# Optimization experiments

Hardware: AMD Instinct MI355X
Metric: run time of the kernel (lower is better)

The kernel has to match this reference:

```python
import jax, jax.numpy as jnp
import numpy as np

N = 200000   # active voxel sites
G = 80       # voxel grid extent per axis
K = 27       # 3x3x3 kernel offsets
CIN = 64
COUT = 128
EPS = 1e-5


def _build_rulebook(seed=0):
    """Submanifold 3x3x3 rulebook: for each offset k and output site i,
    in_idx[k,i] = index of neighbor site (or 0 if absent),
    out_idx[k,i] = i (or N = dummy row if neighbor absent)."""
    rng = np.random.default_rng(seed)
    lin = rng.choice(G ** 3, size=N, replace=False).astype(np.int64)
    lut = np.full(G ** 3, -1, dtype=np.int64)
    lut[lin] = np.arange(N)
    cx, cy, cz = lin // (G * G), (lin // G) % G, lin % G
    offs = [(dx, dy, dz) for dx in (-1, 0, 1) for dy in (-1, 0, 1) for dz in (-1, 0, 1)]
    in_idx = np.zeros((K, N), np.int32)
    out_idx = np.full((K, N), N, np.int32)
    ar = np.arange(N, dtype=np.int32)
    for k, (dx, dy, dz) in enumerate(offs):
        nx, ny, nz = cx + dx, cy + dy, cz + dz
        ok = (nx >= 0) & (nx < G) & (ny >= 0) & (ny < G) & (nz >= 0) & (nz < G)
        nb_lin = np.where(ok, nx * G * G + ny * G + nz, 0)
        j = lut[nb_lin]
        valid = ok & (j >= 0)
        in_idx[k] = np.where(valid, j, 0).astype(np.int32)
        out_idx[k] = np.where(valid, ar, N)
    return jnp.asarray(in_idx), jnp.asarray(out_idx)


def setup_inputs() -> dict:
    key = jax.random.key(0)
    ks = jax.random.split(key, 8)
    in_idx, out_idx = _build_rulebook(0)
    s1 = 1.0 / np.sqrt(CIN * K)
    s2 = 1.0 / np.sqrt(COUT * K)
    ss = 1.0 / np.sqrt(CIN)
    return {
        "feats": jax.random.normal(ks[0], (N, CIN), jnp.float32),
        "in_idx": in_idx,
        "out_idx": out_idx,
        "W1": jax.random.normal(ks[1], (K, CIN, COUT), jnp.float32) * s1,
        "g1": jnp.ones((COUT,), jnp.float32) + 0.1 * jax.random.normal(ks[2], (COUT,), jnp.float32),
        "b1": 0.1 * jax.random.normal(ks[3], (COUT,), jnp.float32),
        "W2": jax.random.normal(ks[4], (K, COUT, COUT), jnp.float32) * s2,
        "g2": jnp.ones((COUT,), jnp.float32) + 0.1 * jax.random.normal(ks[5], (COUT,), jnp.float32),
        "b2": 0.1 * jax.random.normal(ks[6], (COUT,), jnp.float32),
        "Wsc": jax.random.normal(ks[7], (CIN, COUT), jnp.float32) * ss,
        "gsc": jnp.ones((COUT,), jnp.float32),
        "bsc": jnp.zeros((COUT,), jnp.float32),
    }


def _spconv(feats, W, in_idx, out_idx):
    """Rulebook gather-GEMM-scatter sparse conv. feats [N,Cin], W [K,Cin,Cout]."""
    cout = W.shape[-1]
    out = jnp.zeros((N + 1, cout), feats.dtype)  # row N = dummy for padded pairs
    for k in range(K):  # fixed small structural loop over kernel offsets
        out = out.at[out_idx[k]].add(feats[in_idx[k]] @ W[k])
    return out[:N]


def _bn(x, gamma, beta):
    # training-mode BatchNorm over the site dimension (biased variance)
    m = jnp.mean(x, axis=0)
    v = jnp.var(x, axis=0)
    return (x - m) * jax.lax.rsqrt(v + EPS) * gamma + beta


def reference(feats, in_idx, out_idx, W1, g1, b1, W2, g2, b2, Wsc, gsc, bsc):
    h = jax.nn.relu(_bn(_spconv(feats, W1, in_idx, out_idx), g1, b1))
    h = _bn(_spconv(h, W2, in_idx, out_idx), g2, b2)
    sc = _bn(feats @ Wsc, gsc, bsc)  # 1x1 sparse conv == per-site linear
    return jax.nn.relu(h + sc)
```

## Files before the change

kernel.cpp:

```cpp
#include <hip/hip_runtime.h>

#define NS 200000
#define NK 27
#define NB 782
#define NBSC 1563
#define EPSV 1e-5f

typedef __bf16 bf16x8 __attribute__((ext_vector_type(8)));
typedef float f32x4 __attribute__((ext_vector_type(4)));
typedef unsigned short u16;
typedef u16 u16x8 __attribute__((ext_vector_type(8)));
typedef u16 u16x4 __attribute__((ext_vector_type(4)));
typedef unsigned u32;

__device__ __forceinline__ u16 f2bf(float f) {
  union { float f; unsigned u; } v; v.f = f;
  unsigned r = v.u + 0x7fffu + ((v.u >> 16) & 1u);
  return (u16)(r >> 16);
}
__device__ __forceinline__ float bf2f(u16 u) {
  union { unsigned u; float f; } v; v.u = ((unsigned)u) << 16;
  return v.f;
}

__global__ void k_prep_all(const float* __restrict__ feats,
                           const int* __restrict__ in_idx, const int* __restrict__ out_idx,
                           const float* __restrict__ W1, const float* __restrict__ W2,
                           const float* __restrict__ Wsc,
                           u16* __restrict__ Xbf, int* __restrict__ gidx,
                           u16* __restrict__ Wp1, u16* __restrict__ Wp2,
                           u16* __restrict__ Wpsc, float* __restrict__ stats) {
  long i = (long)blockIdx.x * 256 + threadIdx.x;
  if (i < 768) stats[i] = 0.f;
  if (i < (long)NS * 64) Xbf[i] = f2bf(feats[i]);
  if (i < (long)NK * NS) gidx[i] = (out_idx[i] != NS) ? in_idx[i] : NS;
  const int n1 = NK * 64 * 128, n2 = NK * 128 * 128, n3 = 64 * 128;
  if (i < (long)(n1 + n2 + n3)) {
    int ii = (int)i;
    const float* src; u16* dst; int f, S, C;
    if (ii < n1)           { src = W1;  dst = Wp1;  f = ii;           S = 2; C = 64; }
    else if (ii < n1 + n2) { src = W2;  dst = Wp2;  f = ii - n1;      S = 4; C = 128; }
    else                   { src = Wsc; dst = Wpsc; f = ii - n1 - n2; S = 2; C = 64; }
    int j = f & 7, l = (f >> 3) & 63, cf = (f >> 9) & 7;
    int rest = f >> 12;
    int s = rest % S, k = rest / S;
    int kk = s * 32 + (l >> 4) * 8 + j;
    dst[f] = f2bf(src[(k * C + kk) * 128 + cf * 16 + (l & 15)]);
  }
}

template <int C>
__global__ __launch_bounds__(256, 2) void k_conv(
    const u16* __restrict__ X, const u16* __restrict__ Wp,
    const int* __restrict__ gidx,
    u16* __restrict__ Y, float* __restrict__ partial) {
  constexpr int S = C / 32;
  constexpr int SLICE = C * 128;
  constexpr int NST = C / 16;
  constexpr int WAITN = NST + 4;
  __shared__ alignas(16) u16 Wbuf[2 * SLICE];
  __shared__ float red[1024];

  const int t = threadIdx.x, w = t >> 6, l = t & 63;
  const int lr = l & 15, lh = l >> 4;
  const int rowbase = blockIdx.x * 256 + w * 64;
  const int laneoff = l * 8;

  int rc[4]; bool ok[4];
  #pragma unroll
  for (int m = 0; m < 4; ++m) {
    int r = rowbase + m * 16 + lr;
    ok[m] = r < NS;
    rc[m] = ok[m] ? r : 0;
  }

  auto stage = [&](int k, int p) {
    #pragma unroll
    for (int i = 0; i < NST; ++i) {
      const u16* g = Wp + k * SLICE + (w * NST + i) * 512 + laneoff;
      u16* d = &Wbuf[p * SLICE + (w * NST + i) * 512];
      __builtin_amdgcn_global_load_lds(
          (const __attribute__((address_space(1))) u32*)g,
          (__attribute__((address_space(3))) u32*)d, 16, 0, 0);
    }
  };
  auto loadidx = [&](int k, int (&dst)[4]) {
    #pragma unroll
    for (int m = 0; m < 4; ++m) {
      int v = gidx[k * NS + rc[m]];
      dst[m] = ok[m] ? v : NS;
    }
  };
  auto gather = [&](const int (&src)[4], bf16x8 (&a)[4][S]) {
    #pragma unroll
    for (int m = 0; m < 4; ++m) {
      #pragma unroll
      for (int s = 0; s < S; ++s) a[m][s] = bf16x8{};
      if (src[m] != NS) {
        const u16* rowp = X + src[m] * C + lh * 8;
        #pragma unroll
        for (int s = 0; s < S; ++s)
          a[m][s] = *reinterpret_cast<const bf16x8*>(rowp + s * 32);
      }
    }
  };
  auto compute = [&](int p, const bf16x8 (&a)[4][S], f32x4 (&ac)[4][8]) {
    __builtin_amdgcn_s_setprio(1);
    #pragma unroll
    for (int s = 0; s < S; ++s)
      #pragma unroll
      for (int cf = 0; cf < 8; ++cf) {
        bf16x8 b = *reinterpret_cast<const bf16x8*>(
            &Wbuf[p * SLICE + (s * 8 + cf) * 512 + laneoff]);
        #pragma unroll
        for (int m = 0; m < 4; ++m)
          ac[m][cf] = __builtin_amdgcn_mfma_f32_16x16x32_bf16(a[m][s], b, ac[m][cf], 0, 0, 0);
      }
    __builtin_amdgcn_s_setprio(0);
  };

  f32x4 acc[4][8];
  #pragma unroll
  for (int m = 0; m < 4; ++m)
    #pragma unroll
    for (int cf = 0; cf < 8; ++cf) acc[m][cf] = (f32x4){0.f, 0.f, 0.f, 0.f};

  bf16x8 av[4][S];
  int sv0[4], sv1[4];

  loadidx(0, sv0);
  stage(0, 0);
  loadidx(1, sv1);
  gather(sv0, av);

  #pragma unroll 1
  for (int k = 0; k < NK - 1; k += 2) {
    stage(k + 1, 1);
    loadidx(k + 2, sv0);
    asm volatile("s_waitcnt vmcnt(%0)\n\ts_barrier" :: "i"(WAITN) : "memory");
    compute(0, av, acc);
    gather(sv1, av);
    asm volatile("s_waitcnt lgkmcnt(0)\n\ts_barrier" ::: "memory");
    stage(k + 2, 0);
    { int kn = (k + 3 < NK) ? k + 3 : NK - 1; loadidx(kn, sv1); }
    asm volatile("s_waitcnt vmcnt(%0)\n\ts_barrier" :: "i"(WAITN) : "memory");
    compute(1, av, acc);
    gather(sv0, av);
    asm volatile("s_waitcnt lgkmcnt(0)\n\ts_barrier" ::: "memory");
  }
  asm volatile("s_waitcnt vmcnt(0)\n\ts_barrier" ::: "memory");
  compute(0, av, acc);

  #pragma unroll
  for (int m = 0; m < 4; ++m)
    #pragma unroll
    for (int cf = 0; cf < 8; ++cf) {
      int ch = cf * 16 + lr;
      #pragma unroll
      for (int r = 0; r < 4; ++r) {
        int row = rowbase + m * 16 + lh * 4 + r;
        if (row < NS) Y[row * 128 + ch] = f2bf(acc[m][cf][r]);
      }
    }
  #pragma unroll
  for (int cf = 0; cf < 8; ++cf) {
    float s = 0.f, q = 0.f;
    #pragma unroll
    for (int m = 0; m < 4; ++m)
      #pragma unroll
      for (int r = 0; r < 4; ++r) { float v = acc[m][cf][r]; s += v; q += v * v; }
    s += __shfl_xor(s, 16); s += __shfl_xor(s, 32);
    q += __shfl_xor(q, 16); q += __shfl_xor(q, 32);
    if (lh == 0) {
      red[w * 256 + cf * 16 + lr] = s;
      red[w * 256 + 128 + cf * 16 + lr] = q;
    }
  }
  __syncthreads();
  if (t < 256)
    partial[blockIdx.x * 256 + t] =
        red[t] + red[256 + t] + red[512 + t] + red[768 + t];
}

__global__ __launch_bounds__(256, 2) void k_sc(
    const u16* __restrict__ X, const u16* __restrict__ Wpsc,
    u16* __restrict__ SCb, float* __restrict__ partial) {
  __shared__ float red[1024];
  const int t = threadIdx.x, w = t >> 6, l = t & 63;
  const int lr = l & 15, lh = l >> 4;
  const int rowbase = blockIdx.x * 128 + w * 32;
  const int laneoff = l * 8;

  bf16x8 ai[2][2];
  #pragma unroll
  for (int m = 0; m < 2; ++m) {
    int r = rowbase + m * 16 + lr;
    #pragma unroll
    for (int s = 0; s < 2; ++s) ai[m][s] = bf16x8{};
    if (r < NS) {
      const u16* rowp = X + r * 64 + lh * 8;
      ai[m][0] = *reinterpret_cast<const bf16x8*>(rowp);
      ai[m][1] = *reinterpret_cast<const bf16x8*>(rowp + 32);
    }
  }
  f32x4 acc[2][8];
  #pragma unroll
  for (int m = 0; m < 2; ++m)
    #pragma unroll
    for (int cf = 0; cf < 8; ++cf) acc[m][cf] = (f32x4){0.f, 0.f, 0.f, 0.f};
  #pragma unroll
  for (int s = 0; s < 2; ++s)
    #pragma unroll
    for (int cf = 0; cf < 8; ++cf) {
      bf16x8 b = *reinterpret_cast<const bf16x8*>(Wpsc + (s * 8 + cf) * 512 + laneoff);
      acc[0][cf] = __builtin_amdgcn_mfma_f32_16x16x32_bf16(ai[0][s], b, acc[0][cf], 0, 0, 0);
      acc[1][cf] = __builtin_amdgcn_mfma_f32_16x16x32_bf16(ai[1][s], b, acc[1][cf], 0, 0, 0);
    }
  #pragma unroll
  for (int m = 0; m < 2; ++m)
    #pragma unroll
    for (int cf = 0; cf < 8; ++cf) {
      int ch = cf * 16 + lr;
      #pragma unroll
      for (int r = 0; r < 4; ++r) {
        int row = rowbase + m * 16 + lh * 4 + r;
        if (row < NS) SCb[row * 128 + ch] = f2bf(acc[m][cf][r]);
      }
    }
  #pragma unroll
  for (int cf = 0; cf < 8; ++cf) {
    float s = 0.f, q = 0.f;
    #pragma unroll
    for (int m = 0; m < 2; ++m)
      #pragma unroll
      for (int r = 0; r < 4; ++r) { float v = acc[m][cf][r]; s += v; q += v * v; }
    s += __shfl_xor(s, 16); s += __shfl_xor(s, 32);
    q += __shfl_xor(q, 16); q += __shfl_xor(q, 32);
    if (lh == 0) {
      red[w * 256 + cf * 16 + lr] = s;
      red[w * 256 + 128 + cf * 16 + lr] = q;
    }
  }
  __syncthreads();
  if (t < 256)
    partial[(long)blockIdx.x * 256 + t] =
        red[t] + red[256 + t] + red[512 + t] + red[768 + t];
}

__global__ void k_red1x2(const float* __restrict__ pa, const float* __restrict__ pb,
                         float* __restrict__ tmp) {
  int c = threadIdx.x;
  const float* p = (blockIdx.x == 0) ? pa : pb;
  int nrows = (blockIdx.x == 0) ? NB : NBSC;
  int roff  = (blockIdx.x == 0) ? 0 : 256;
  float s = 0.f;
  for (int r = blockIdx.y; r < nrows; r += 32) s += p[(long)r * 256 + c];
  tmp[(long)blockIdx.y * 512 + roff + c] = s;
}
__global__ void k_red1(const float* __restrict__ part, float* __restrict__ tmp,
                       int nrows) {
  int c = threadIdx.x;
  float s = 0.f;
  for (int r = blockIdx.y; r < nrows; r += 32) s += part[(long)r * 256 + c];
  tmp[(long)blockIdx.y * 512 + c] = s;
}
__global__ void k_red2(const float* __restrict__ tmp, float* __restrict__ out) {
  int c = blockIdx.x * 256 + threadIdx.x;
  float s = 0.f;
  #pragma unroll
  for (int r = 0; r < 32; ++r) s += tmp[(long)r * 512 + c];
  out[c] = s;
}

__global__ void k_bnrelu(const u16* __restrict__ Y1, const float* __restrict__ stats,
                         const float* __restrict__ g, const float* __restrict__ b,
                         u16* __restrict__ H) {
  long i8 = (long)blockIdx.x * 256 + threadIdx.x;
  const long tot = (long)NS * 16;
  if (i8 >= tot) return;
  int ch0 = ((int)i8 & 15) * 8;
  u16x8 y = *reinterpret_cast<const u16x8*>(Y1 + i8 * 8);
  u16x8 o;
  #pragma unroll
  for (int e = 0; e < 8; ++e) {
    int ch = ch0 + e;
    float m = stats[ch] * (1.f / NS);
    float var = stats[128 + ch] * (1.f / NS) - m * m;
    float a = g[ch] * rsqrtf(var + EPSV);
    float bb = b[ch] - m * a;
    float h = bf2f(y[e]) * a + bb;
    o[e] = f2bf(h > 0.f ? h : 0.f);
  }
  *reinterpret_cast<u16x8*>(H + i8 * 8) = o;
}

__global__ void k_final(const u16* __restrict__ Y2, const u16* __restrict__ SCb,
                        const float* __restrict__ stats,
                        const float* __restrict__ g2, const float* __restrict__ b2,
                        const float* __restrict__ gsc, const float* __restrict__ bsc,
                        float* __restrict__ out) {
  long i8 = (long)blockIdx.x * 256 + threadIdx.x;
  if (i8 >= (long)NS * 16) return;
  int ch0 = ((int)i8 & 15) * 8;
  u16x8 y = *reinterpret_cast<const u16x8*>(Y2 + i8 * 8);
  u16x8 s = *reinterpret_cast<const u16x8*>(SCb + i8 * 8);
  f32x4 o0, o1;
  #pragma unroll
  for (int e = 0; e < 8; ++e) {
    int ch = ch0 + e;
    float m2 = stats[512 + ch] * (1.f / NS);
    float v2 = stats[640 + ch] * (1.f / NS) - m2 * m2;
    float a2 = g2[ch] * rsqrtf(v2 + EPSV);
    float msc = stats[256 + ch] * (1.f / NS);
    float vsc = stats[384 + ch] * (1.f / NS) - msc * msc;
    float asc = gsc[ch] * rsqrtf(vsc + EPSV);
    float val = bf2f(y[e]) * a2 + (b2[ch] - m2 * a2)
              + bf2f(s[e]) * asc + (bsc[ch] - msc * asc);
    float rv = val > 0.f ? val : 0.f;
    if (e < 4) o0[e] = rv; else o1[e - 4] = rv;
  }
  *reinterpret_cast<f32x4*>(out + i8 * 8) = o0;
  *reinterpret_cast<f32x4*>(out + i8 * 8 + 4) = o1;
}

extern "C" void kernel_launch(void* const* d_in, const int* in_sizes, int n_in,
                              void* d_out, int out_size, void* d_ws, size_t ws_size,
                              hipStream_t stream) {
  const float* feats = (const float*)d_in[0];
  const int* in_idx  = (const int*)d_in[1];
  const int* out_idx = (const int*)d_in[2];
  const float* W1  = (const float*)d_in[3];
  const float* g1  = (const float*)d_in[4];
  const float* b1  = (const float*)d_in[5];
  const float* W2  = (const float*)d_in[6];
  const float* g2  = (const float*)d_in[7];
  const float* b2  = (const float*)d_in[8];
  const float* Wsc = (const float*)d_in[9];
  const float* gsc = (const float*)d_in[10];
  const float* bsc = (const float*)d_in[11];

  char* ws = (char*)d_ws;
  size_t off = 0;
  auto alloc = [&](size_t bytes) {
    void* p = ws + off; off += (bytes + 255) & ~(size_t)255; return p;
  };
  float* stats = (float*)alloc(768 * 4);
  float* rtmp  = (float*)alloc(32 * 512 * 4);
  u16* Xbf  = (u16*)alloc((size_t)NS * 64 * 2);
  u16* SCbf = (u16*)alloc((size_t)NS * 128 * 2);
  u16* Hbf  = (u16*)alloc((size_t)NS * 128 * 2);
  u16* Y2bf = (u16*)alloc((size_t)NS * 128 * 2);
  u16* Wp1  = (u16*)alloc((size_t)NK * 64 * 128 * 2);
  u16* Wp2  = (u16*)alloc((size_t)NK * 128 * 128 * 2);
  u16* Wpsc = (u16*)alloc((size_t)64 * 128 * 2);
  u16* Y1bf = (u16*)d_out;
  int* gidx = (int*)((char*)d_out + (size_t)NS * 128 * 2);
  float* part1  = (float*)Y2bf;
  float* partsc = part1 + (size_t)NB * 256;
  float* part2  = (float*)Xbf;

  hipLaunchKernelGGL(k_prep_all, dim3(50000), dim3(256), 0, stream,
                     feats, in_idx, out_idx, W1, W2, Wsc,
                     Xbf, gidx, Wp1, Wp2, Wpsc, stats);
  hipLaunchKernelGGL(k_sc, dim3(NBSC), dim3(256), 0, stream, Xbf, Wpsc, SCbf, partsc);
  hipLaunchKernelGGL((k_conv<64>), dim3(NB), dim3(256), 0, stream,
                     Xbf, Wp1, gidx, Y1bf, part1);
  hipLaunchKernelGGL(k_red1x2, dim3(2, 32), dim3(256), 0, stream, part1, partsc, rtmp);
  hipLaunchKernelGGL(k_red2, dim3(2), dim3(256), 0, stream, rtmp, stats);
  hipLaunchKernelGGL(k_bnrelu, dim3(12500), dim3(256), 0, stream, Y1bf, stats, g1, b1, Hbf);
  hipLaunchKernelGGL((k_conv<128>), dim3(NB), dim3(256), 0, stream,
                     Hbf, Wp2, gidx, Y2bf, part2);
  hipLaunchKernelGGL(k_red1, dim3(1, 32), dim3(256), 0, stream, part2, rtmp, NB);
  hipLaunchKernelGGL(k_red2, dim3(1), dim3(256), 0, stream, rtmp, stats + 512);
  hipLaunchKernelGGL(k_final, dim3(12500), dim3(256), 0, stream,
                     Y2bf, SCbf, stats, g2, b2, gsc, bsc, (float*)d_out);
}
```

Measured before the change: 421.4 us.

## Stage gathered activation rows into LDS via async loads with 2D warp tiling

The sparse conv kernel now gathers neighbor rows straight into a swizzled LDS buffer with global_load_lds, double-buffered with the weights, so gathers no longer go through registers. Blocks grow to 512 threads over 128 rows, and each wave owns a 64x32 output tile (wm/wn split), which shrinks accumulator registers and allows more occupancy. Absent neighbors now point to a zeroed dummy row NS in X and H instead of being masked per lane, which needs extra padding rows and tail handling. The added LDS use and the new synchronization pattern may limit the occupancy this is meant to gain.

```diff
diff --git a/kernel.cpp b/kernel.cpp
--- a/kernel.cpp
+++ b/kernel.cpp
@@ -2,15 +2,13 @@
 
 #define NS 200000
 #define NK 27
-#define NB 782
-#define NBSC 1563
+#define NB 1563
 #define EPSV 1e-5f
 
 typedef __bf16 bf16x8 __attribute__((ext_vector_type(8)));
 typedef float f32x4 __attribute__((ext_vector_type(4)));
 typedef unsigned short u16;
 typedef u16 u16x8 __attribute__((ext_vector_type(8)));
-typedef u16 u16x4 __attribute__((ext_vector_type(4)));
 typedef unsigned u32;
 
 __device__ __forceinline__ u16 f2bf(float f) {
@@ -32,6 +30,7 @@
                            u16* __restrict__ Wpsc, float* __restrict__ stats) {
   long i = (long)blockIdx.x * 256 + threadIdx.x;
   if (i < 768) stats[i] = 0.f;
+  if (i < 64 && blockIdx.x == 0) Xbf[(long)NS * 64 + i] = (u16)0;
   if (i < (long)NS * 64) Xbf[i] = f2bf(feats[i]);
   if (i < (long)NK * NS) gidx[i] = (out_idx[i] != NS) ? in_idx[i] : NS;
   const int n1 = NK * 64 * 128, n2 = NK * 128 * 128, n3 = 64 * 128;
@@ -50,136 +49,148 @@
 }
 
 template <int C>
-__global__ __launch_bounds__(256, 2) void k_conv(
+__global__ __launch_bounds__(512, (C == 64) ? 4 : 2) void k_conv(
     const u16* __restrict__ X, const u16* __restrict__ Wp,
     const int* __restrict__ gidx,
     u16* __restrict__ Y, float* __restrict__ partial) {
   constexpr int S = C / 32;
-  constexpr int SLICE = C * 128;
-  constexpr int NST = C / 16;
-  constexpr int WAITN = NST + 4;
-  __shared__ alignas(16) u16 Wbuf[2 * SLICE];
-  __shared__ float red[1024];
+  constexpr int UA = C / 8;
+  constexpr int LUA = (C == 64) ? 3 : 4;
+  constexpr int ASL = 128 * UA * 8;
+  constexpr int WSL = C * 128;
+  constexpr int NIT = (C == 64) ? 2 : 4;
+  constexpr int RPI = 512 >> LUA;
+  constexpr int WAITN = 3 * NIT;
+  __shared__ alignas(16) u16 Wbuf[2 * WSL];
+  __shared__ alignas(16) u16 Abuf[2 * ASL];
+  __shared__ float red[512];
 
   const int t = threadIdx.x, w = t >> 6, l = t & 63;
   const int lr = l & 15, lh = l >> 4;
-  const int rowbase = blockIdx.x * 256 + w * 64;
-  const int laneoff = l * 8;
-
-  int rc[4]; bool ok[4];
-  #pragma unroll
-  for (int m = 0; m < 4; ++m) {
-    int r = rowbase + m * 16 + lr;
-    ok[m] = r < NS;
-    rc[m] = ok[m] ? r : 0;
-  }
-
-  auto stage = [&](int k, int p) {
-    #pragma unroll
-    for (int i = 0; i < NST; ++i) {
-      const u16* g = Wp + k * SLICE + (w * NST + i) * 512 + laneoff;
-      u16* d = &Wbuf[p * SLICE + (w * NST + i) * 512];
+  const int wm = w >> 2, wn = w & 3;
+  const int rowblk = blockIdx.x * 128;
+
+  auto stageW = [&](int k, int p) {
+    #pragma unroll
+    for (int i = 0; i < NIT; ++i) {
+      const u16* g = Wp + (long)k * WSL + (i * 512 + t) * 8;
+      u16* d = &Wbuf[p * WSL + (i * 512 + t) * 8];
       __builtin_amdgcn_global_load_lds(
           (const __attribute__((address_space(1))) u32*)g,
           (__attribute__((address_space(3))) u32*)d, 16, 0, 0);
     }
   };
-  auto loadidx = [&](int k, int (&dst)[4]) {
-    #pragma unroll
-    for (int m = 0; m < 4; ++m) {
-      int v = gidx[k * NS + rc[m]];
-      dst[m] = ok[m] ? v : NS;
-    }
-  };
-  auto gather = [&](const int (&src)[4], bf16x8 (&a)[4][S]) {
-    #pragma unroll
-    for (int m = 0; m < 4; ++m) {
-      #pragma unroll
-      for (int s = 0; s < S; ++s) a[m][s] = bf16x8{};
-      if (src[m] != NS) {
-        const u16* rowp = X + src[m] * C + lh * 8;
-        #pragma unroll
-        for (int s = 0; s < S; ++s)
-          a[m][s] = *reinterpret_cast<const bf16x8*>(rowp + s * 32);
+  auto loadidx = [&](int k, int (&iv)[NIT]) {
+    #pragma unroll
+    for (int i = 0; i < NIT; ++i) {
+      int rg = rowblk + i * RPI + (t >> LUA);
+      bool okr = rg < NS;
+      int v = gidx[(long)k * NS + (okr ? rg : 0)];
+      iv[i] = okr ? v : NS;
+    }
+  };
+  auto stageA = [&](int p, const int (&iv)[NIT]) {
+    #pragma unroll
+    for (int i = 0; i < NIT; ++i) {
+      int rloc = i * RPI + (t >> LUA);
+      int c = t & (UA - 1);
+      int csw = c ^ (rloc & 7);
+      const u16* g = X + (long)iv[i] * C + csw * 8;
+      u16* d = &Abuf[p * ASL + ((i * 512 + t) * 8)];
+      __builtin_amdgcn_global_load_lds(
+          (const __attribute__((address_space(1))) u32*)g,
+          (__attribute__((address_space(3))) u32*)d, 16, 0, 0);
+    }
+  };
+  auto compute = [&](int p, f32x4 (&ac)[4][2]) {
+    __builtin_amdgcn_s_setprio(1);
+    #pragma unroll
+    for (int s = 0; s < S; ++s) {
+      bf16x8 a[4];
+      #pragma unroll
+      for (int m = 0; m < 4; ++m) {
+        int row = wm * 64 + m * 16 + lr;
+        int unit = row * UA + ((s * 4 + lh) ^ (row & 7));
+        a[m] = *reinterpret_cast<const bf16x8*>(&Abuf[p * ASL + unit * 8]);
       }
-    }
-  };
-  auto compute = [&](int p, const bf16x8 (&a)[4][S], f32x4 (&ac)[4][8]) {
-    __builtin_amdgcn_s_setprio(1);
-    #pragma unroll
-    for (int s = 0; s < S; ++s)
-      #pragma unroll
-      for (int cf = 0; cf < 8; ++cf) {
+      #pragma unroll
+      for (int nf = 0; nf < 2; ++nf) {
         bf16x8 b = *reinterpret_cast<const bf16x8*>(
-            &Wbuf[p * SLICE + (s * 8 + cf) * 512 + laneoff]);
+            &Wbuf[p * WSL + (s * 8 + wn * 2 + nf) * 512 + l * 8]);
         #pragma unroll
         for (int m = 0; m < 4; ++m)
-          ac[m][cf] = __builtin_amdgcn_mfma_f32_16x16x32_bf16(a[m][s], b, ac[m][cf], 0, 0, 0);
+          ac[m][nf] = __builtin_amdgcn_mfma_f32_16x16x32_bf16(a[m], b, ac[m][nf], 0, 0, 0);
       }
+    }
     __builtin_amdgcn_s_setprio(0);
   };
 
-  f32x4 acc[4][8];
+  f32x4 acc[4][2];
   #pragma unroll
   for (int m = 0; m < 4; ++m)
     #pragma unroll
-    for (int cf = 0; cf < 8; ++cf) acc[m][cf] = (f32x4){0.f, 0.f, 0.f, 0.f};
-
-  bf16x8 av[4][S];
-  int sv0[4], sv1[4];
+    for (int nf = 0; nf < 2; ++nf) acc[m][nf] = (f32x4){0.f, 0.f, 0.f, 0.f};
+
+  int sv0[NIT], sv1[NIT];
 
   loadidx(0, sv0);
-  stage(0, 0);
   loadidx(1, sv1);
-  gather(sv0, av);
+  stageW(0, 0);
+  asm volatile("s_waitcnt vmcnt(%0)" :: "i"(2 * NIT) : "memory");
+  stageA(0, sv0);
 
   #pragma unroll 1
   for (int k = 0; k < NK - 1; k += 2) {
-    stage(k + 1, 1);
+    stageW(k + 1, 1);
     loadidx(k + 2, sv0);
+    asm volatile("s_waitcnt vmcnt(%0)" :: "i"(WAITN) : "memory");
+    stageA(1, sv1);
     asm volatile("s_waitcnt vmcnt(%0)\n\ts_barrier" :: "i"(WAITN) : "memory");
-    compute(0, av, acc);
-    gather(sv1, av);
+    compute(0, acc);
     asm volatile("s_waitcnt lgkmcnt(0)\n\ts_barrier" ::: "memory");
-    stage(k + 2, 0);
+    stageW(k + 2, 0);
     { int kn = (k + 3 < NK) ? k + 3 : NK - 1; loadidx(kn, sv1); }
+    asm volatile("s_waitcnt vmcnt(%0)" :: "i"(WAITN) : "memory");
+    stageA(0, sv0);
     asm volatile("s_waitcnt vmcnt(%0)\n\ts_barrier" :: "i"(WAITN) : "memory");
-    compute(1, av, acc);
-    gather(sv0, av);
+    compute(1, acc);
     asm volatile("s_waitcnt lgkmcnt(0)\n\ts_barrier" ::: "memory");
   }
   asm volatile("s_waitcnt vmcnt(0)\n\ts_barrier" ::: "memory");
-  compute(0, av, acc);
+  compute(0, acc);
 
   #pragma unroll
   for (int m = 0; m < 4; ++m)
     #pragma unroll
-    for (int cf = 0; cf < 8; ++cf) {
-      int ch = cf * 16 + lr;
+    for (int nf = 0; nf < 2; ++nf) {
+      int ch = wn * 32 + nf * 16 + lr;
       #pragma unroll
       for (int r = 0; r < 4; ++r) {
-        int row = rowbase + m * 16 + lh * 4 + r;
-        if (row < NS) Y[row * 128 + ch] = f2bf(acc[m][cf][r]);
+        int row = rowblk + wm * 64 + m * 16 + lh * 4 + r;
+        if (row < NS) Y[(long)row * 128 + ch] = f2bf(acc[m][nf][r]);
       }
     }
   #pragma unroll
-  for (int cf = 0; cf < 8; ++cf) {
+  for (int nf = 0; nf < 2; ++nf) {
     float s = 0.f, q = 0.f;
     #pragma unroll
     for (int m = 0; m < 4; ++m)
       #pragma unroll
-      for (int r = 0; r < 4; ++r) { float v = acc[m][cf][r]; s += v; q += v * v; }
+      for (int r = 0; r < 4; ++r) { float v = acc[m][nf][r]; s += v; q += v * v; }
     s += __shfl_xor(s, 16); s += __shfl_xor(s, 32);
     q += __shfl_xor(q, 16); q += __shfl_xor(q, 32);
     if (lh == 0) {
-      red[w * 256 + cf * 16 + lr] = s;
-      red[w * 256 + 128 + cf * 16 + lr] = q;
+      red[w * 64 + nf * 16 + lr] = s;
+      red[w * 64 + 32 + nf * 16 + lr] = q;
     }
   }
   __syncthreads();
-  if (t < 256)
-    partial[blockIdx.x * 256 + t] =
-        red[t] + red[256 + t] + red[512 + t] + red[768 + t];
+  if (t < 256) {
+    int isq = t >> 7, c = t & 127;
+    int wnc = c >> 5, c31 = c & 31;
+    partial[(long)blockIdx.x * 256 + t] =
+        red[wnc * 64 + isq * 32 + c31] + red[(4 + wnc) * 64 + isq * 32 + c31];
+  }
 }
 
 __global__ __launch_bounds__(256, 2) void k_sc(
@@ -198,7 +209,7 @@
     #pragma unroll
     for (int s = 0; s < 2; ++s) ai[m][s] = bf16x8{};
     if (r < NS) {
-      const u16* rowp = X + r * 64 + lh * 8;
+      const u16* rowp = X + (long)r * 64 + lh * 8;
       ai[m][0] = *reinterpret_cast<const bf16x8*>(rowp);
       ai[m][1] = *reinterpret_cast<const bf16x8*>(rowp + 32);
     }
@@ -224,7 +235,7 @@
       #pragma unroll
       for (int r = 0; r < 4; ++r) {
         int row = rowbase + m * 16 + lh * 4 + r;
-        if (row < NS) SCb[row * 128 + ch] = f2bf(acc[m][cf][r]);
+        if (row < NS) SCb[(long)row * 128 + ch] = f2bf(acc[m][cf][r]);
       }
     }
   #pragma unroll
@@ -251,17 +262,15 @@
                          float* __restrict__ tmp) {
   int c = threadIdx.x;
   const float* p = (blockIdx.x == 0) ? pa : pb;
-  int nrows = (blockIdx.x == 0) ? NB : NBSC;
-  int roff  = (blockIdx.x == 0) ? 0 : 256;
+  int roff = (blockIdx.x == 0) ? 0 : 256;
   float s = 0.f;
-  for (int r = blockIdx.y; r < nrows; r += 32) s += p[(long)r * 256 + c];
+  for (int r = blockIdx.y; r < NB; r += 32) s += p[(long)r * 256 + c];
   tmp[(long)blockIdx.y * 512 + roff + c] = s;
 }
-__global__ void k_red1(const float* __restrict__ part, float* __restrict__ tmp,
-                       int nrows) {
+__global__ void k_red1(const float* __restrict__ part, float* __restrict__ tmp) {
   int c = threadIdx.x;
   float s = 0.f;
-  for (int r = blockIdx.y; r < nrows; r += 32) s += part[(long)r * 256 + c];
+  for (int r = blockIdx.y; r < NB; r += 32) s += part[(long)r * 256 + c];
   tmp[(long)blockIdx.y * 512 + c] = s;
 }
 __global__ void k_red2(const float* __restrict__ tmp, float* __restrict__ out) {
@@ -276,20 +285,26 @@
                          const float* __restrict__ g, const float* __restrict__ b,
                          u16* __restrict__ H) {
   long i8 = (long)blockIdx.x * 256 + threadIdx.x;
-  const long tot = (long)NS * 16;
+  const long tot = (long)(NS + 1) * 16;
   if (i8 >= tot) return;
-  int ch0 = ((int)i8 & 15) * 8;
-  u16x8 y = *reinterpret_cast<const u16x8*>(Y1 + i8 * 8);
+  long row = i8 >> 4;
   u16x8 o;
-  #pragma unroll
-  for (int e = 0; e < 8; ++e) {
-    int ch = ch0 + e;
-    float m = stats[ch] * (1.f / NS);
-    float var = stats[128 + ch] * (1.f / NS) - m * m;
-    float a = g[ch] * rsqrtf(var + EPSV);
-    float bb = b[ch] - m * a;
-    float h = bf2f(y[e]) * a + bb;
-    o[e] = f2bf(h > 0.f ? h : 0.f);
+  if (row < NS) {
+    int ch0 = ((int)i8 & 15) * 8;
+    u16x8 y = *reinterpret_cast<const u16x8*>(Y1 + i8 * 8);
+    #pragma unroll
+    for (int e = 0; e < 8; ++e) {
+      int ch = ch0 + e;
+      float m = stats[ch] * (1.f / NS);
+      float var = stats[128 + ch] * (1.f / NS) - m * m;
+      float a = g[ch] * rsqrtf(var + EPSV);
+      float bb = b[ch] - m * a;
+      float h = bf2f(y[e]) * a + bb;
+      o[e] = f2bf(h > 0.f ? h : 0.f);
+    }
+  } else {
+    #pragma unroll
+    for (int e = 0; e < 8; ++e) o[e] = (u16)0;
   }
   *reinterpret_cast<u16x8*>(H + i8 * 8) = o;
 }
@@ -346,9 +361,9 @@
   };
   float* stats = (float*)alloc(768 * 4);
   float* rtmp  = (float*)alloc(32 * 512 * 4);
-  u16* Xbf  = (u16*)alloc((size_t)NS * 64 * 2);
+  u16* Xbf  = (u16*)alloc((size_t)(NS + 1) * 64 * 2);
   u16* SCbf = (u16*)alloc((size_t)NS * 128 * 2);
-  u16* Hbf  = (u16*)alloc((size_t)NS * 128 * 2);
+  u16* Hbf  = (u16*)alloc((size_t)(NS + 1) * 128 * 2);
   u16* Y2bf = (u16*)alloc((size_t)NS * 128 * 2);
   u16* Wp1  = (u16*)alloc((size_t)NK * 64 * 128 * 2);
   u16* Wp2  = (u16*)alloc((size_t)NK * 128 * 128 * 2);
@@ -362,15 +377,15 @@
   hipLaunchKernelGGL(k_prep_all, dim3(50000), dim3(256), 0, stream,
                      feats, in_idx, out_idx, W1, W2, Wsc,
                      Xbf, gidx, Wp1, Wp2, Wpsc, stats);
-  hipLaunchKernelGGL(k_sc, dim3(NBSC), dim3(256), 0, stream, Xbf, Wpsc, SCbf, partsc);
-  hipLaunchKernelGGL((k_conv<64>), dim3(NB), dim3(256), 0, stream,
+  hipLaunchKernelGGL(k_sc, dim3(NB), dim3(256), 0, stream, Xbf, Wpsc, SCbf, partsc);
+  hipLaunchKernelGGL((k_conv<64>), dim3(NB), dim3(512), 0, stream,
                      Xbf, Wp1, gidx, Y1bf, part1);
   hipLaunchKernelGGL(k_red1x2, dim3(2, 32), dim3(256), 0, stream, part1, partsc, rtmp);
   hipLaunchKernelGGL(k_red2, dim3(2), dim3(256), 0, stream, rtmp, stats);
-  hipLaunchKernelGGL(k_bnrelu, dim3(12500), dim3(256), 0, stream, Y1bf, stats, g1, b1, Hbf);
-  hipLaunchKernelGGL((k_conv<128>), dim3(NB), dim3(256), 0, stream,
+  hipLaunchKernelGGL(k_bnrelu, dim3(12501), dim3(256), 0, stream, Y1bf, stats, g1, b1, Hbf);
+  hipLaunchKernelGGL((k_conv<128>), dim3(NB), dim3(512), 0, stream,
                      Hbf, Wp2, gidx, Y2bf, part2);
-  hipLaunchKernelGGL(k_red1, dim3(1, 32), dim3(256), 0, stream, part2, rtmp, NB);
+  hipLaunchKernelGGL(k_red1, dim3(1, 32), dim3(256), 0, stream, part2, rtmp);
   hipLaunchKernelGGL(k_red2, dim3(1), dim3(256), 0, stream, rtmp, stats + 512);
   hipLaunchKernelGGL(k_final, dim3(12500), dim3(256), 0, stream,
                      Y2bf, SCbf, stats, g2, b2, gsc, bsc, (float*)d_out);
```

New measurement: 544.9 us. +29.3%, slower.
